# Kernel optimization log

Measured on AMD Instinct MI355X. Metric: run time of the kernel, lower is better.

Reference implementation:

```python
import jax, jax.numpy as jnp
import numpy as np

H = 256   # encoder/decoder hidden size
U = 128   # attention units


def setup_inputs() -> dict:
    key = jax.random.key(0)
    ks = jax.random.split(key, 8)
    B, Td, Te = 16, 128, 1024
    s = 1.0 / np.sqrt(H)
    return {
        "dec_outputs": jax.random.normal(ks[0], (B, Td, H), dtype=jnp.float32),
        "enc_outputs": jax.random.normal(ks[1], (B, Te, H), dtype=jnp.float32),
        "W1": jax.random.normal(ks[2], (H, U), dtype=jnp.float32) * s,
        "b1": jnp.zeros((U,), dtype=jnp.float32),
        "W2": jax.random.normal(ks[3], (H, U), dtype=jnp.float32) * s,
        "b2": jnp.zeros((U,), dtype=jnp.float32),
        "V": jax.random.normal(ks[4], (U, 1), dtype=jnp.float32) * (1.0 / np.sqrt(U)),
        "bv": jnp.zeros((1,), dtype=jnp.float32),
    }


def reference(dec_outputs, enc_outputs, W1, b1, W2, b2, V, bv):
    # Project once (the original redundantly re-projects enc_outputs per step).
    # w1d: [B, Td, U], w2e: [B, Te, U]
    w1d = jnp.einsum("bth,hu->btu", dec_outputs, W1) + b1
    w2e = jnp.einsum("bsh,hu->bsu", enc_outputs, W2) + b2
    # Additive Bahdanau score: tanh over broadcast sum -> [B, Td, Te, U]
    feat = jnp.tanh(w1d[:, :, None, :] + w2e[:, None, :, :])
    # V projection to scalar score: [B, Td, Te]
    score = jnp.einsum("btsu,u->bts", feat, V[:, 0]) + bv[0]
    # Softmax over encoder positions (original Softmax(axis=1) on [B, Te])
    return jax.nn.softmax(score, axis=-1)
```

## Files before the change

kernel.cpp:

```cpp
#include <hip/hip_runtime.h>
#include <math.h>

#define HB 256
#define UB 128
#define BB 16
#define TD 128
#define TE 1024

#define CLAMP_W 7.0f
#define L2E2 2.8853900817779268f
#define ALPHA 1.52587890625e-05f
#define NEG2ALPHA (-3.0517578125e-05f)

#define PINV(x) asm volatile("" : "+v"(x))
#define PINS(x) asm volatile("" : "+s"(x))
#define PINV4(q) do { PINV((q).x); PINV((q).y); PINV((q).z); PINV((q).w); } while (0)
#define PINS4(q) do { PINS((q).x); PINS((q).y); PINS((q).z); PINS((q).w); } while (0)

__device__ __forceinline__ float stage_exp(float w, float shift) {
    float t = fminf(fmaxf(w, -CLAMP_W), CLAMP_W);
    return exp2f(fmaf(t, L2E2, shift));
}

#define DEC_SLABS 32
#define NSLABS 288
#define PROJ_BLOCKS (NSLABS * 2)

__global__ __launch_bounds__(512) void proj_v13(
    const float* __restrict__ dec, const float* __restrict__ enc,
    const float* __restrict__ W1, const float* __restrict__ b1,
    const float* __restrict__ W2, const float* __restrict__ b2,
    float* __restrict__ Ea, float* __restrict__ Eb) {
    const int blk = blockIdx.x;
    const int slab = blk >> 1, uhalf = blk & 1;
    const bool is_dec = slab < DEC_SLABS;
    const int rel = is_dec ? slab : slab - DEC_SLABS;
    const float* __restrict__ X    = is_dec ? dec : enc;
    const float* __restrict__ W    = is_dec ? W1 : W2;
    const float* __restrict__ bias = is_dec ? b1 : b2;

    __shared__ float xt[HB][66];
    const int tid = threadIdx.x;
    const long row0 = (long)rel * 64;

    #pragma unroll
    for (int it = 0; it < 8; ++it) {
        int idx = it * 512 + tid;
        int row = idx >> 6, hf4 = idx & 63;
        float4 f = *reinterpret_cast<const float4*>(X + (row0 + row) * HB + hf4 * 4);
        xt[hf4 * 4 + 0][row] = f.x;
        xt[hf4 * 4 + 1][row] = f.y;
        xt[hf4 * 4 + 2][row] = f.z;
        xt[hf4 * 4 + 3][row] = f.w;
    }
    __syncthreads();

    const int l = tid & 63;
    const int w = __builtin_amdgcn_readfirstlane(tid >> 6);
    const int ub3 = w & 3;
    const int ub  = ub3 + uhalf * 4;
    const int hh  = w >> 2;
    const int u0  = ub * 16;
    const int h0  = hh * 128;

    float acc[16];
    #pragma unroll
    for (int j = 0; j < 16; ++j) acc[j] = 0.f;

    float4 wfC[4][4], wfN[4][4];
    float  xkC[4], xkN[4];
    #pragma unroll
    for (int k = 0; k < 4; ++k) {
        #pragma unroll
        for (int q = 0; q < 4; ++q)
            wfC[k][q] = *reinterpret_cast<const float4*>(W + (h0 + k) * UB + u0 + q * 4);
        xkC[k] = xt[h0 + k][l];
    }

    for (int h = 0; h < 128; h += 4) {
        const int hg = h0 + h;
        const int hn = (h + 4 < 128) ? hg + 4 : h0;
        #pragma unroll
        for (int k = 0; k < 4; ++k) {
            #pragma unroll
            for (int q = 0; q < 4; ++q)
                wfN[k][q] = *reinterpret_cast<const float4*>(W + (hn + k) * UB + u0 + q * 4);
            xkN[k] = xt[hn + k][l];
        }
        #pragma unroll
        for (int k = 0; k < 4; ++k)
            #pragma unroll
            for (int q = 0; q < 4; ++q) {
                acc[q * 4 + 0] = fmaf(xkC[k], wfC[k][q].x, acc[q * 4 + 0]);
                acc[q * 4 + 1] = fmaf(xkC[k], wfC[k][q].y, acc[q * 4 + 1]);
                acc[q * 4 + 2] = fmaf(xkC[k], wfC[k][q].z, acc[q * 4 + 2]);
                acc[q * 4 + 3] = fmaf(xkC[k], wfC[k][q].w, acc[q * 4 + 3]);
            }
        #pragma unroll
        for (int k = 0; k < 4; ++k) {
            PINS4(wfN[k][0]); PINS4(wfN[k][1]); PINS4(wfN[k][2]); PINS4(wfN[k][3]);
            PINV(xkN[k]);
        }
        #pragma unroll
        for (int k = 0; k < 4; ++k) {
            #pragma unroll
            for (int q = 0; q < 4; ++q) wfC[k][q] = wfN[k][q];
            xkC[k] = xkN[k];
        }
    }

    __syncthreads();
    float4* red = reinterpret_cast<float4*>(&xt[0][0]);
    if (hh == 1) {
        #pragma unroll
        for (int q = 0; q < 4; ++q)
            red[((ub3 * 64 + l) << 2) + q] =
                make_float4(acc[q * 4], acc[q * 4 + 1], acc[q * 4 + 2], acc[q * 4 + 3]);
    }
    __syncthreads();
    if (hh == 0) {
        #pragma unroll
        for (int q = 0; q < 4; ++q) {
            float4 r = red[((ub3 * 64 + l) << 2) + q];
            acc[q * 4 + 0] += r.x; acc[q * 4 + 1] += r.y;
            acc[q * 4 + 2] += r.z; acc[q * 4 + 3] += r.w;
        }
        const float sh = is_dec ? -16.f : 0.f;
        const int POS  = is_dec ? TD : TE;
        const long bq  = row0 / POS;
        const int pos  = (int)(row0 % POS) + l;
        float4* dst4 = reinterpret_cast<float4*>(is_dec ? Ea : Eb);
        #pragma unroll
        for (int q = 0; q < 4; ++q) {
            float4 o = make_float4(
                stage_exp(acc[q * 4 + 0] + bias[u0 + q * 4 + 0], sh),
                stage_exp(acc[q * 4 + 1] + bias[u0 + q * 4 + 1], sh),
                stage_exp(acc[q * 4 + 2] + bias[u0 + q * 4 + 2], sh),
                stage_exp(acc[q * 4 + 3] + bias[u0 + q * 4 + 3], sh));
            dst4[(bq * 32 + ub * 4 + q) * (long)POS + pos] = o;
        }
    }
}

__global__ __launch_bounds__(1024) void score_v13(
    const float* __restrict__ Ea4,
    const float4* __restrict__ Eb4,
    const float* __restrict__ V,
    float* __restrict__ out) {
    const int tid = threadIdx.x;
    const int wv = tid >> 6, l = tid & 63;
    const int i = blockIdx.x;
    const int b  = 2 * (i & 7) + ((i >> 3) >> 4);
    const int t0 = ((i >> 3) & 15) * 8;

    const float*  ab = Ea4 + ((long)b * 32 * TD) * 4;
    const float4* ep = Eb4 + (long)b * 32 * TE + tid;
    const float alphav = ALPHA;

    float acc[8];
    #pragma unroll
    for (int t = 0; t < 8; ++t) acc[t] = 0.f;

    float4 aC[8], aN[8], vC, vN, e0, e1, e2;
#define ALOAD(AB, VB, U4) do {                                            \
        const float* _a = ab + ((long)(U4) * TD + t0) * 4;                \
        _Pragma("unroll")                                                 \
        for (int t = 0; t < 8; ++t)                                       \
            AB[t] = *reinterpret_cast<const float4*>(_a + t * 4);         \
        VB = *reinterpret_cast<const float4*>(V + (U4) * 4);              \
    } while (0)

#define SCOMP(AB, VB, EB) do {                                            \
        _Pragma("unroll")                                                 \
        for (int t = 0; t < 8; ++t) {                                     \
            float4 A = AB[t];                                             \
            float X0 = fmaf(A.x, (EB).x, alphav);                         \
            float X1 = fmaf(A.y, (EB).y, alphav);                         \
            float X2 = fmaf(A.z, (EB).z, alphav);                         \
            float X3 = fmaf(A.w, (EB).w, alphav);                         \
            float P01 = X0 * X1, P23 = X2 * X3;                           \
            float N01 = fmaf((VB).x, X1, (VB).y * X0);                    \
            float N23 = fmaf((VB).z, X3, (VB).w * X2);                    \
            float N   = fmaf(N01, P23, N23 * P01);                        \
            acc[t] = fmaf(N, __builtin_amdgcn_rcpf(P01 * P23), acc[t]);   \
        }                                                                 \
    } while (0)

    ALOAD(aC, vC, 0);
    e0 = ep[0];
    e1 = ep[TE];
    #pragma unroll 2
    for (int u4 = 0; u4 < 32; ++u4) {
        const int p1 = (u4 + 1 < 32) ? u4 + 1 : 0;
        const int p2 = (u4 + 2 < 32) ? u4 + 2 : 0;
        e2 = ep[(long)p2 * TE];
        ALOAD(aN, vN, p1);
        SCOMP(aC, vC, e0);
        #pragma unroll
        for (int t = 0; t < 8; ++t) PINS4(aN[t]);
        PINS4(vN);
        PINV4(e2);
        #pragma unroll
        for (int t = 0; t < 8; ++t) aC[t] = aN[t];
        vC = vN;
        e0 = e1; e1 = e2;
    }
#undef ALOAD
#undef SCOMP

    float sc[8];
    #pragma unroll
    for (int t = 0; t < 8; ++t) sc[t] = NEG2ALPHA * acc[t];

    __shared__ float red[8][16];
    #pragma unroll
    for (int t = 0; t < 8; ++t) {
        float x = sc[t];
        #pragma unroll
        for (int off = 32; off > 0; off >>= 1) x = fmaxf(x, __shfl_xor(x, off, 64));
        if (l == 0) red[t][wv] = x;
    }
    __syncthreads();
    float m[8];
    #pragma unroll
    for (int t = 0; t < 8; ++t) {
        float x = red[t][0];
        #pragma unroll
        for (int k = 1; k < 16; ++k) x = fmaxf(x, red[t][k]);
        m[t] = x;
    }
    __syncthreads();
    #pragma unroll
    for (int t = 0; t < 8; ++t) {
        sc[t] = __expf(sc[t] - m[t]);
        float x = sc[t];
        #pragma unroll
        for (int off = 32; off > 0; off >>= 1) x += __shfl_xor(x, off, 64);
        if (l == 0) red[t][wv] = x;
    }
    __syncthreads();
    #pragma unroll
    for (int t = 0; t < 8; ++t) {
        float x = red[t][0];
        #pragma unroll
        for (int k = 1; k < 16; ++k) x += red[t][k];
        out[((long)b * TD + t0 + t) * TE + tid] = sc[t] * (1.f / x);
    }
}

extern "C" void kernel_launch(void* const* d_in, const int* in_sizes, int n_in,
                              void* d_out, int out_size, void* d_ws, size_t ws_size,
                              hipStream_t stream) {
    const float* dec = (const float*)d_in[0];
    const float* enc = (const float*)d_in[1];
    const float* W1  = (const float*)d_in[2];
    const float* b1  = (const float*)d_in[3];
    const float* W2  = (const float*)d_in[4];
    const float* b2  = (const float*)d_in[5];
    const float* V   = (const float*)d_in[6];
    float* out = (float*)d_out;

    float* Ea = (float*)d_ws;
    float* Eb = Ea + (long)BB * 32 * TD * 4;

    proj_v13<<<PROJ_BLOCKS, 512, 0, stream>>>(dec, enc, W1, b1, W2, b2, Ea, Eb);
    score_v13<<<256, 1024, 0, stream>>>(Ea, (const float4*)Eb, V, out);
}
```

Before: 67.57 us.

## Use split-bf16 MFMA for projection GEMM with finer unit tiling

Replaces the fp32 FMA projection kernel with a bf16 MFMA kernel that splits inputs and weights into high/low bf16 parts to approximate fp32 accuracy via three MFMAs. Each block now handles 16 attention units for a 64-row slab, with the slab converted into shared memory. This aims to cut projection compute time, but each input slab is reloaded by eight blocks and precision is slightly below full fp32.

New measurement: 70.25 us. 4.0% more time.

```diff
diff --git a/kernel.cpp b/kernel.cpp
--- a/kernel.cpp
+++ b/kernel.cpp
@@ -17,128 +17,106 @@
 #define PINV4(q) do { PINV((q).x); PINV((q).y); PINV((q).z); PINV((q).w); } while (0)
 #define PINS4(q) do { PINS((q).x); PINS((q).y); PINS((q).z); PINS((q).w); } while (0)
 
+typedef __attribute__((ext_vector_type(8))) short bf16x8;
+typedef __attribute__((ext_vector_type(4))) float f32x4;
+
+__device__ __forceinline__ unsigned short f2bf(float x) {
+    union { float f; unsigned u; } v; v.f = x;
+    unsigned r = v.u + 0x7FFFu + ((v.u >> 16) & 1u);
+    return (unsigned short)(r >> 16);
+}
+__device__ __forceinline__ float bf2f(unsigned short h) {
+    union { float f; unsigned u; } v; v.u = ((unsigned)h) << 16;
+    return v.f;
+}
+
 __device__ __forceinline__ float stage_exp(float w, float shift) {
     float t = fminf(fmaxf(w, -CLAMP_W), CLAMP_W);
     return exp2f(fmaf(t, L2E2, shift));
 }
 
-#define DEC_SLABS 32
-#define NSLABS 288
-#define PROJ_BLOCKS (NSLABS * 2)
-
-__global__ __launch_bounds__(512) void proj_v13(
+#define SLABS 288
+#define PROJ_BLOCKS (SLABS * 8)
+
+__global__ __launch_bounds__(256) void proj_mfma(
     const float* __restrict__ dec, const float* __restrict__ enc,
     const float* __restrict__ W1, const float* __restrict__ b1,
     const float* __restrict__ W2, const float* __restrict__ b2,
     float* __restrict__ Ea, float* __restrict__ Eb) {
-    const int blk = blockIdx.x;
-    const int slab = blk >> 1, uhalf = blk & 1;
-    const bool is_dec = slab < DEC_SLABS;
-    const int rel = is_dec ? slab : slab - DEC_SLABS;
+    const int bid  = blockIdx.x;
+    const int slab = bid >> 3;
+    const int ut   = bid & 7;
+    const bool is_dec = slab < 32;
+    const int rel = is_dec ? slab : slab - 32;
     const float* __restrict__ X    = is_dec ? dec : enc;
     const float* __restrict__ W    = is_dec ? W1 : W2;
     const float* __restrict__ bias = is_dec ? b1 : b2;
 
-    __shared__ float xt[HB][66];
+    __shared__ unsigned short xh[64][264];
+    __shared__ unsigned short xl[64][264];
+
     const int tid = threadIdx.x;
     const long row0 = (long)rel * 64;
 
     #pragma unroll
-    for (int it = 0; it < 8; ++it) {
-        int idx = it * 512 + tid;
-        int row = idx >> 6, hf4 = idx & 63;
-        float4 f = *reinterpret_cast<const float4*>(X + (row0 + row) * HB + hf4 * 4);
-        xt[hf4 * 4 + 0][row] = f.x;
-        xt[hf4 * 4 + 1][row] = f.y;
-        xt[hf4 * 4 + 2][row] = f.z;
-        xt[hf4 * 4 + 3][row] = f.w;
-    }
-    __syncthreads();
-
-    const int l = tid & 63;
-    const int w = __builtin_amdgcn_readfirstlane(tid >> 6);
-    const int ub3 = w & 3;
-    const int ub  = ub3 + uhalf * 4;
-    const int hh  = w >> 2;
-    const int u0  = ub * 16;
-    const int h0  = hh * 128;
-
-    float acc[16];
-    #pragma unroll
-    for (int j = 0; j < 16; ++j) acc[j] = 0.f;
-
-    float4 wfC[4][4], wfN[4][4];
-    float  xkC[4], xkN[4];
-    #pragma unroll
-    for (int k = 0; k < 4; ++k) {
-        #pragma unroll
-        for (int q = 0; q < 4; ++q)
-            wfC[k][q] = *reinterpret_cast<const float4*>(W + (h0 + k) * UB + u0 + q * 4);
-        xkC[k] = xt[h0 + k][l];
-    }
-
-    for (int h = 0; h < 128; h += 4) {
-        const int hg = h0 + h;
-        const int hn = (h + 4 < 128) ? hg + 4 : h0;
-        #pragma unroll
-        for (int k = 0; k < 4; ++k) {
-            #pragma unroll
-            for (int q = 0; q < 4; ++q)
-                wfN[k][q] = *reinterpret_cast<const float4*>(W + (hn + k) * UB + u0 + q * 4);
-            xkN[k] = xt[hn + k][l];
+    for (int it = 0; it < 16; ++it) {
+        int idx = it * 256 + tid;
+        int r = idx >> 6, c4 = idx & 63;
+        float4 f = *reinterpret_cast<const float4*>(X + (row0 + r) * HB + c4 * 4);
+        unsigned short h0 = f2bf(f.x), h1 = f2bf(f.y), h2 = f2bf(f.z), h3 = f2bf(f.w);
+        *reinterpret_cast<ushort4*>(&xh[r][c4 * 4]) = make_ushort4(h0, h1, h2, h3);
+        unsigned short l0 = f2bf(f.x - bf2f(h0)), l1 = f2bf(f.y - bf2f(h1));
+        unsigned short l2 = f2bf(f.z - bf2f(h2)), l3 = f2bf(f.w - bf2f(h3));
+        *reinterpret_cast<ushort4*>(&xl[r][c4 * 4]) = make_ushort4(l0, l1, l2, l3);
+    }
+
+    const int l  = tid & 63;
+    const int wv = tid >> 6;
+    const int ucol = ut * 16 + (l & 15);
+    const int kg = (l >> 4) * 8;
+
+    bf16x8 bh[8], bl[8];
+    #pragma unroll
+    for (int s = 0; s < 8; ++s) {
+        const float* wp = W + (32 * s + kg) * UB + ucol;
+        short hb[8], lb[8];
+        #pragma unroll
+        for (int j = 0; j < 8; ++j) {
+            float w = wp[j * UB];
+            unsigned short h = f2bf(w);
+            hb[j] = (short)h;
+            lb[j] = (short)f2bf(w - bf2f(h));
         }
-        #pragma unroll
-        for (int k = 0; k < 4; ++k)
-            #pragma unroll
-            for (int q = 0; q < 4; ++q) {
-                acc[q * 4 + 0] = fmaf(xkC[k], wfC[k][q].x, acc[q * 4 + 0]);
-                acc[q * 4 + 1] = fmaf(xkC[k], wfC[k][q].y, acc[q * 4 + 1]);
-                acc[q * 4 + 2] = fmaf(xkC[k], wfC[k][q].z, acc[q * 4 + 2]);
-                acc[q * 4 + 3] = fmaf(xkC[k], wfC[k][q].w, acc[q * 4 + 3]);
-            }
-        #pragma unroll
-        for (int k = 0; k < 4; ++k) {
-            PINS4(wfN[k][0]); PINS4(wfN[k][1]); PINS4(wfN[k][2]); PINS4(wfN[k][3]);
-            PINV(xkN[k]);
-        }
-        #pragma unroll
-        for (int k = 0; k < 4; ++k) {
-            #pragma unroll
-            for (int q = 0; q < 4; ++q) wfC[k][q] = wfN[k][q];
-            xkC[k] = xkN[k];
-        }
-    }
-
-    __syncthreads();
-    float4* red = reinterpret_cast<float4*>(&xt[0][0]);
-    if (hh == 1) {
-        #pragma unroll
-        for (int q = 0; q < 4; ++q)
-            red[((ub3 * 64 + l) << 2) + q] =
-                make_float4(acc[q * 4], acc[q * 4 + 1], acc[q * 4 + 2], acc[q * 4 + 3]);
-    }
-    __syncthreads();
-    if (hh == 0) {
-        #pragma unroll
-        for (int q = 0; q < 4; ++q) {
-            float4 r = red[((ub3 * 64 + l) << 2) + q];
-            acc[q * 4 + 0] += r.x; acc[q * 4 + 1] += r.y;
-            acc[q * 4 + 2] += r.z; acc[q * 4 + 3] += r.w;
-        }
-        const float sh = is_dec ? -16.f : 0.f;
-        const int POS  = is_dec ? TD : TE;
-        const long bq  = row0 / POS;
-        const int pos  = (int)(row0 % POS) + l;
-        float4* dst4 = reinterpret_cast<float4*>(is_dec ? Ea : Eb);
-        #pragma unroll
-        for (int q = 0; q < 4; ++q) {
-            float4 o = make_float4(
-                stage_exp(acc[q * 4 + 0] + bias[u0 + q * 4 + 0], sh),
-                stage_exp(acc[q * 4 + 1] + bias[u0 + q * 4 + 1], sh),
-                stage_exp(acc[q * 4 + 2] + bias[u0 + q * 4 + 2], sh),
-                stage_exp(acc[q * 4 + 3] + bias[u0 + q * 4 + 3], sh));
-            dst4[(bq * 32 + ub * 4 + q) * (long)POS + pos] = o;
-        }
+        bh[s] = (bf16x8){hb[0], hb[1], hb[2], hb[3], hb[4], hb[5], hb[6], hb[7]};
+        bl[s] = (bf16x8){lb[0], lb[1], lb[2], lb[3], lb[4], lb[5], lb[6], lb[7]};
+    }
+    __syncthreads();
+
+    f32x4 acc0 = {0.f, 0.f, 0.f, 0.f};
+    f32x4 acc1 = {0.f, 0.f, 0.f, 0.f};
+    f32x4 acc2 = {0.f, 0.f, 0.f, 0.f};
+    const int arow = wv * 16 + (l & 15);
+
+    #pragma unroll
+    for (int s = 0; s < 8; ++s) {
+        bf16x8 ah = *reinterpret_cast<const bf16x8*>(&xh[arow][32 * s + kg]);
+        bf16x8 al = *reinterpret_cast<const bf16x8*>(&xl[arow][32 * s + kg]);
+        acc0 = __builtin_amdgcn_mfma_f32_16x16x32_bf16(ah, bh[s], acc0, 0, 0, 0);
+        acc1 = __builtin_amdgcn_mfma_f32_16x16x32_bf16(ah, bl[s], acc1, 0, 0, 0);
+        acc2 = __builtin_amdgcn_mfma_f32_16x16x32_bf16(al, bh[s], acc2, 0, 0, 0);
+    }
+
+    const float bv = bias[ucol];
+    const float sh = is_dec ? -16.f : 0.f;
+    const int POS  = is_dec ? TD : TE;
+    const long bq  = row0 / POS;
+    const int posb = (int)(row0 % POS) + wv * 16 + (l >> 4) * 4;
+    float* __restrict__ dst = is_dec ? Ea : Eb;
+    const long ubase = (bq * 32 + (ucol >> 2)) * (long)POS;
+    #pragma unroll
+    for (int q = 0; q < 4; ++q) {
+        float v = acc0[q] + acc1[q] + acc2[q] + bv;
+        dst[(ubase + posb + q) * 4 + (ucol & 3)] = stage_exp(v, sh);
     }
 }
 
@@ -263,6 +241,6 @@
     float* Ea = (float*)d_ws;
     float* Eb = Ea + (long)BB * 32 * TD * 4;
 
-    proj_v13<<<PROJ_BLOCKS, 512, 0, stream>>>(dec, enc, W1, b1, W2, b2, Ea, Eb);
+    proj_mfma<<<PROJ_BLOCKS, 256, 0, stream>>>(dec, enc, W1, b1, W2, b2, Ea, Eb);
     score_v13<<<256, 1024, 0, stream>>>(Ea, (const float4*)Eb, V, out);
 }
```
